# Performance work log

Hardware: AMD Instinct MI355X
Metric: run time of the kernel (lower is better)

Reference implementation:

```python
import jax, jax.numpy as jnp
import numpy as np

B, N, T, D, H, NE = 8, 128, 49, 4, 256, 2  # batch, nodes, timesteps, dims, hidden, edge types


def _mlp(x, w1, b1, w2, b2):
    # NRI-style 2-layer MLP with ELU activations (dropout=0, batch_norm off)
    h = jax.nn.elu(x @ w1 + b1)
    return jax.nn.elu(h @ w2 + b2)


def setup_inputs() -> dict:
    key = jax.random.key(0)
    ks = jax.random.split(key, 11)
    # fully-connected graph without self loops -> E = N*(N-1)
    off = ~np.eye(N, dtype=bool)
    recv_idx, send_idx = np.nonzero(off)
    eye = np.eye(N, dtype=np.float32)
    rec_rel = jnp.asarray(eye[recv_idx])   # [E, N] one-hot receivers
    send_rel = jnp.asarray(eye[send_idx])  # [E, N] one-hot senders
    x = jax.random.normal(ks[0], (B, N, T, D), jnp.float32)

    def lin(k, fi, fo):
        kw, kb = jax.random.split(k)
        return (0.02 * jax.random.normal(kw, (fi, fo), jnp.float32),
                0.02 * jax.random.normal(kb, (fo,), jnp.float32))

    F = T * D
    n1w1, n1b1 = lin(ks[1], F, H)
    n1w2, n1b2 = lin(ks[2], H, H)
    e1w1, e1b1 = lin(ks[3], 2 * H, H)
    e1w2, e1b2 = lin(ks[4], H, H)
    n2w1, n2b1 = lin(ks[5], H, H)
    n2w2, n2b2 = lin(ks[6], H, H)
    e2w1, e2b1 = lin(ks[7], 3 * H, H)
    e2w2, e2b2 = lin(ks[8], H, H)
    ow, ob = lin(ks[9], H, NE)
    return dict(x=x, rec_rel=rec_rel, send_rel=send_rel,
                n1w1=n1w1, n1b1=n1b1, n1w2=n1w2, n1b2=n1b2,
                e1w1=e1w1, e1b1=e1b1, e1w2=e1w2, e1b2=e1b2,
                n2w1=n2w1, n2b1=n2b1, n2w2=n2w2, n2b2=n2b2,
                e2w1=e2w1, e2b1=e2b1, e2w2=e2w2, e2b2=e2b2,
                ow=ow, ob=ob)


def reference(x, rec_rel, send_rel,
              n1w1, n1b1, n1w2, n1b2,
              e1w1, e1b1, e1w2, e1b2,
              n2w1, n2b1, n2w2, n2b2,
              e2w1, e2b1, e2w2, e2b2,
              ow, ob):
    b, n = x.shape[0], x.shape[1]
    h = x.reshape(b, n, -1)                         # [B, N, T*D]
    h = _mlp(h, n1w1, n1b1, n1w2, n1b2)             # node_emd 1 -> [B, N, H]
    r = jnp.einsum('en,bnf->bef', rec_rel, h)       # gather receivers [B, E, H]
    s = jnp.einsum('en,bnf->bef', send_rel, h)      # gather senders  [B, E, H]
    e = _mlp(jnp.concatenate([r, s], -1), e1w1, e1b1, e1w2, e1b2)  # edge_emd 1
    x_skip = e                                      # '@' skip connection
    agg = jnp.einsum('en,bef->bnf', rec_rel, e)     # aggregate sum -> [B, N, H]
    h = _mlp(agg, n2w1, n2b1, n2w2, n2b2)           # node_emd 2
    r = jnp.einsum('en,bnf->bef', rec_rel, h)
    s = jnp.einsum('en,bnf->bef', send_rel, h)
    e = jnp.concatenate([r, s, x_skip], -1)         # pairwise concat + residual cat
    e = _mlp(e, e2w1, e2b1, e2w2, e2b2)             # edge_emd 2 (final)
    return e @ ow + ob                              # [B, E, n_edge_types]
```

## Files before the change

kernel.cpp:

```cpp
#include <hip/hip_runtime.h>
#include <hip/hip_bf16.h>

typedef unsigned short ushort_t;
typedef short bf16x8 __attribute__((ext_vector_type(8)));
typedef float f32x4 __attribute__((ext_vector_type(4)));

#define B_ 8
#define N_ 128
#define E_ 16256
#define BE 130048

__device__ __forceinline__ float eluf(float x) {
    return x > 0.0f ? x : __expf(x) - 1.0f;
}
__device__ __forceinline__ ushort_t f2bf(float f) {
    union { float f; unsigned u; } v; v.f = f;
    return (ushort_t)((v.u + 0x7fffu + ((v.u >> 16) & 1u)) >> 16);
}
__device__ __forceinline__ float bf2f(ushort_t h) {
    union { unsigned u; float f; } v; v.u = ((unsigned)h) << 16;
    return v.f;
}

__device__ __forceinline__ void glds16(void* lds, const void* g) {
    __builtin_amdgcn_global_load_lds(
        (const __attribute__((address_space(1))) unsigned int*)g,
        (__attribute__((address_space(3))) unsigned int*)lds, 16, 0, 0);
}

__device__ __forceinline__ void img32_elem(const float* __restrict__ w,
                                           ushort_t* __restrict__ img, int i) {
    int c = i >> 13;  int r = i & 8191;
    int n = r >> 5;   int jq = r & 31;
    int quad = jq >> 3, j = jq & 7;
    int kc = quad ^ ((n >> 1) & 3);
    int k = c * 32 + kc * 8 + j;
    img[i] = f2bf(w[(size_t)k * 256 + n]);
}
__device__ __forceinline__ void img128_elem(const float* __restrict__ w,
                                            ushort_t* __restrict__ img, int i) {
    int c = i >> 15;  int r = i & 32767;
    int n = r >> 7;   int wdx = r & 127;
    int up = wdx >> 3, j = wdx & 7;
    int u = up ^ (n & 15);
    int k = c * 128 + u * 8 + j;
    img[i] = f2bf(w[(size_t)k * 256 + n]);
}
__device__ __forceinline__ void img128_pad(const float* __restrict__ w,
                                           ushort_t* __restrict__ img, int i, int Kreal) {
    int c = i >> 15;  int r = i & 32767;
    int n = r >> 7;   int wdx = r & 127;
    int up = wdx >> 3, j = wdx & 7;
    int u = up ^ (n & 15);
    int k = c * 128 + u * 8 + j;
    img[i] = (k < Kreal) ? f2bf(w[(size_t)k * 256 + n]) : (ushort_t)0;
}

__global__ __launch_bounds__(256) void wprep_all(
    const float* __restrict__ n1w1, ushort_t* __restrict__ s0,
    const float* __restrict__ n1w2, ushort_t* __restrict__ s1,
    const float* __restrict__ e1w1, ushort_t* __restrict__ s2, ushort_t* __restrict__ s3,
    const float* __restrict__ n2w1, ushort_t* __restrict__ s4,
    const float* __restrict__ n2w2, ushort_t* __restrict__ s5,
    const float* __restrict__ e2w1, ushort_t* __restrict__ s6, ushort_t* __restrict__ s7,
    ushort_t* __restrict__ s8,
    const float* __restrict__ e1w2, ushort_t* __restrict__ s9,
    const float* __restrict__ e2w2, ushort_t* __restrict__ s10)
{
    int gid = blockIdx.x * 256 + threadIdx.x;
    int img = gid >> 16, r = gid & 65535;
    switch (img) {
        case 0:  img128_pad (n1w1, s0, r, 196); break;
        case 1:  img128_elem(n1w2, s1, r); break;
        case 2:  img128_elem(e1w1, s2, r); break;
        case 3:  img128_elem(e1w1 + 65536, s3, r); break;
        case 4:  img128_elem(n2w1, s4, r); break;
        case 5:  img128_elem(n2w2, s5, r); break;
        case 6:  img128_elem(e2w1, s6, r); break;
        case 7:  img128_elem(e2w1 + 65536, s7, r); break;
        case 8:  img32_elem (e2w1 + 131072, s8, r); break;
        case 9:  img32_elem (e1w2, s9, r); break;
        default: img32_elem (e2w2, s10, r); break;
    }
}

template<bool TWOIN>
__global__ __launch_bounds__(256, 1) void node_fused(
    const float* __restrict__ in0, const float* __restrict__ in1,
    const ushort_t* __restrict__ iw1, const float* __restrict__ b1,
    const ushort_t* __restrict__ iw2, const float* __restrict__ b2,
    const ushort_t* __restrict__ ipr, const ushort_t* __restrict__ ips,
    const float* __restrict__ bE,
    float* __restrict__ P)
{
    extern __shared__ char smem[];
    const int t = threadIdx.x;
    const int wid = t >> 6, lane = t & 63, lr = lane & 15, lg = lane >> 4;
    const int r0 = blockIdx.x * 32;

    float bias1[4], bias2[4], biasP[4];
    #pragma unroll
    for (int f = 0; f < 4; ++f) {
        int col = wid * 64 + f * 16 + lr;
        bias1[f] = b1[col];
        bias2[f] = b2[col];
        biasP[f] = 0.5f * bE[col];
    }

    f32x4 acc[2][4];
    #pragma unroll
    for (int m = 0; m < 2; ++m)
        #pragma unroll
        for (int f = 0; f < 4; ++f) acc[m][f] = f32x4{0.f, 0.f, 0.f, 0.f};

    auto stageW = [&](const ushort_t* img, int c, int p) {
        const char* src = (const char*)img + (size_t)c * 65536 + wid * 16384 + lane * 16;
        char* dst = smem + 16384 + p * 65536 + wid * 16384;
        #pragma unroll
        for (int it = 0; it < 16; ++it) glds16(dst + it * 1024, src + it * 1024);
    };

    int cc = 0;
    auto runGemm = [&](const ushort_t* img, const ushort_t* nimg) {
        for (int c = 0; c < 2; ++c) {
            const int p = cc & 1;
            if (c + 1 < 2)  stageW(img, 1, p ^ 1);
            else if (nimg)  stageW(nimg, 0, p ^ 1);
            const char* Wp = smem + 16384 + p * 65536;
            #pragma unroll
            for (int ks = 0; ks < 4; ++ks) {
                const int c32 = c * 4 + ks;
                bf16x8 a[2], b[4];
                const int qh = ((c32 * 4 + lg) ^ (lr & 7)) << 4;
                #pragma unroll
                for (int m = 0; m < 2; ++m)
                    a[m] = *(const bf16x8*)(smem + (m * 16 + lr) * 512 + qh);
                #pragma unroll
                for (int f = 0; f < 4; ++f)
                    b[f] = *(const bf16x8*)(Wp + (wid * 64 + f * 16 + lr) * 256 + (((ks * 4 + lg) ^ lr) << 4));
                #pragma unroll
                for (int m = 0; m < 2; ++m)
                    #pragma unroll
                    for (int f = 0; f < 4; ++f)
                        acc[m][f] = __builtin_amdgcn_mfma_f32_16x16x32_bf16(a[m], b[f], acc[m][f], 0, 0, 0);
            }
            __syncthreads();
            ++cc;
        }
    };

    auto transition = [&](const float* bv) {
        #pragma unroll
        for (int m = 0; m < 2; ++m)
            #pragma unroll
            for (int f = 0; f < 4; ++f) {
                const int col = wid * 64 + f * 16 + lr;
                const int ch = col >> 3;
                #pragma unroll
                for (int r = 0; r < 4; ++r) {
                    const int row = m * 16 + lg * 4 + r;
                    float v = eluf(acc[m][f][r] + bv[f]);
                    *(ushort_t*)(smem + row * 512 + ((ch ^ (row & 7)) << 4) + ((col & 7) << 1)) = f2bf(v);
                }
                acc[m][f] = f32x4{0.f, 0.f, 0.f, 0.f};
            }
        __syncthreads();
    };

    auto pwrite = [&](int half) {
        #pragma unroll
        for (int m = 0; m < 2; ++m)
            #pragma unroll
            for (int f = 0; f < 4; ++f) {
                const int col = wid * 64 + f * 16 + lr;
                #pragma unroll
                for (int r = 0; r < 4; ++r) {
                    const int row = m * 16 + lg * 4 + r;
                    P[(size_t)(r0 + row) * 512 + half * 256 + col] = acc[m][f][r] + biasP[f];
                }
                acc[m][f] = f32x4{0.f, 0.f, 0.f, 0.f};
            }
    };

    stageW(iw1, 0, 0);
    for (int idx = t; idx < 32 * 128; idx += 256) {
        const int row = idx >> 7;
        const int c0 = (idx & 127) * 2;
        float v0, v1;
        if (TWOIN) {
            const float* pa = in0 + (size_t)(r0 + row) * 256;
            const float* pb = in1 + (size_t)(r0 + row) * 256;
            v0 = pa[c0] + pb[c0];
            v1 = pa[c0 + 1] + pb[c0 + 1];
        } else {
            const float* pa = in0 + (size_t)(r0 + row) * 196;
            v0 = (c0 < 196) ? pa[c0] : 0.f;
            v1 = (c0 + 1 < 196) ? pa[c0 + 1] : 0.f;
        }
        unsigned u = (unsigned)f2bf(v0) | ((unsigned)f2bf(v1) << 16);
        const int ch = c0 >> 3;
        *(unsigned*)(smem + row * 512 + ((ch ^ (row & 7)) << 4) + (c0 & 7) * 2) = u;
    }
    __syncthreads();

    runGemm(iw1, iw2);
    transition(bias1);
    runGemm(iw2, ipr);
    transition(bias2);
    runGemm(ipr, ips);
    pwrite(0);
    runGemm(ips, nullptr);
    pwrite(1);
}

__global__ __launch_bounds__(512, 2) void edge1_kernel(
    const float* __restrict__ P1,
    const ushort_t* __restrict__ wAimg, const float* __restrict__ biasA,
    const ushort_t* __restrict__ wBimg,
    ushort_t* __restrict__ G1,
    float* __restrict__ aggp0, float* __restrict__ aggp1)
{
    extern __shared__ char smem[];
    const int t = threadIdx.x;
    const int wid = t >> 6, lane = t & 63, lr = lane & 15, lg = lane >> 4;
    const int wr = wid >> 1, wc = wid & 1;
    const int q4 = (lg ^ ((lr >> 1) & 3)) << 4;
    const int blockRow = blockIdx.x * 256;

    auto stageW = [&](const ushort_t* img, int c, int p) {
        const char* src = (const char*)img + (size_t)c * 16384 + wid * 2048 + lane * 16;
        char* dst = smem + 131072 + p * 16384 + wid * 2048;
        glds16(dst, src);
        glds16(dst + 1024, src + 1024);
    };

    float bA[8];
    #pragma unroll
    for (int f = 0; f < 8; ++f) bA[f] = biasA[wc * 128 + f * 16 + lr];

    f32x4 acc[4][8];
    #pragma unroll
    for (int m = 0; m < 4; ++m)
        #pragma unroll
        for (int f = 0; f < 8; ++f) acc[m][f] = f32x4{0.f, 0.f, 0.f, 0.f};

    stageW(wAimg, 0, 0);
    #pragma unroll 4
    for (int j = 0; j < 32; ++j) {
        const int row = wid * 32 + j;
        const int rg = blockRow + row;
        const int b = rg / E_; const int e = rg - b * E_;
        const int rcv = e / 127; const int kk = e - rcv * 127;
        const int snd = kk + (kk >= rcv ? 1 : 0);
        const float4 vr = *(const float4*)(P1 + (size_t)(b * N_ + rcv) * 512 + lane * 4);
        const float4 vs = *(const float4*)(P1 + (size_t)(b * N_ + snd) * 512 + 256 + lane * 4);
        unsigned u0 = (unsigned)f2bf(eluf(vr.x + vs.x)) | ((unsigned)f2bf(eluf(vr.y + vs.y)) << 16);
        unsigned u1 = (unsigned)f2bf(eluf(vr.z + vs.z)) | ((unsigned)f2bf(eluf(vr.w + vs.w)) << 16);
        const int byte = row * 512 + ((((lane >> 1) ^ (row & 7))) << 4) + (lane & 1) * 8;
        *(uint2*)(smem + byte) = make_uint2(u0, u1);
    }
    __syncthreads();

    for (int c = 0; c < 8; ++c) {
        const int p = c & 1;
        if (c < 7) stageW(wAimg, c + 1, p ^ 1);
        else       stageW(wBimg, 0, p ^ 1);
        const char* Wp = smem + 131072 + p * 16384;
        bf16x8 a[4], b[8];
        const int qh = ((c * 4 + lg) ^ (lr & 7)) << 4;
        #pragma unroll
        for (int m = 0; m < 4; ++m)
            a[m] = *(const bf16x8*)(smem + (wr * 64 + m * 16 + lr) * 512 + qh);
        #pragma unroll
        for (int f = 0; f < 8; ++f)
            b[f] = *(const bf16x8*)(Wp + (wc * 128 + f * 16 + lr) * 64 + q4);
        #pragma unroll
        for (int m = 0; m < 4; ++m)
            #pragma unroll
            for (int f = 0; f < 8; ++f)
                acc[m][f] = __builtin_amdgcn_mfma_f32_16x16x32_bf16(a[m], b[f], acc[m][f], 0, 0, 0);
        __syncthreads();
    }

    const int gR0 = blockRow + wr * 64;
    const int sFirst = gR0 / 127;
    const int bk = 127 - (gR0 - sFirst * 127);
    float s0[8], s1[8];
    #pragma unroll
    for (int f = 0; f < 8; ++f) { s0[f] = 0.f; s1[f] = 0.f; }
    #pragma unroll
    for (int m = 0; m < 4; ++m)
        #pragma unroll
        for (int f = 0; f < 8; ++f) {
            const int col = wc * 128 + f * 16 + lr;
            const int ch = col >> 3;
            #pragma unroll
            for (int r = 0; r < 4; ++r) {
                const int rowL = m * 16 + lg * 4 + r;
                const int row = wr * 64 + rowL;
                float v = eluf(acc[m][f][r] + bA[f]);
                *(ushort_t*)(smem + row * 512 + ((ch ^ (row & 7)) << 4) + ((col & 7) << 1)) = f2bf(v);
                if (rowL < bk) s0[f] += v; else s1[f] += v;
            }
            acc[m][f] = f32x4{0.f, 0.f, 0.f, 0.f};
        }
    #pragma unroll
    for (int f = 0; f < 8; ++f) {
        s0[f] += __shfl_xor(s0[f], 16); s0[f] += __shfl_xor(s0[f], 32);
        s1[f] += __shfl_xor(s1[f], 16); s1[f] += __shfl_xor(s1[f], 32);
    }
    float* pt = (float*)(smem + 131072 + 16384);
    if (lg == 0) {
        #pragma unroll
        for (int f = 0; f < 8; ++f) {
            pt[(wid * 2 + 0) * 128 + f * 16 + lr] = s0[f];
            pt[(wid * 2 + 1) * 128 + f * 16 + lr] = s1[f];
        }
    }
    __syncthreads();
    {
        const int S0 = blockRow / 127;
        const int last = (blockRow + 255) / 127;
        const int cnt = last - S0 + 1;
        for (int task = t; task < cnt * 256; task += 512) {
            const int k = task >> 8;
            const int col = task & 255;
            const int sigma = S0 + k;
            const int wcq = col >> 7, c128 = col & 127;
            float sum = 0.f;
            #pragma unroll
            for (int w2r = 0; w2r < 4; ++w2r) {
                int sf = (blockRow + w2r * 64) / 127;
                int jj = sigma - sf;
                if (jj == 0 || jj == 1)
                    sum += pt[((w2r * 2 + wcq) * 2 + jj) * 128 + c128];
            }
            const bool startIn = (127 * sigma >= blockRow);
            const bool endIn = (127 * sigma + 127 <= blockRow + 256);
            if (startIn) {
                aggp0[(size_t)sigma * 256 + col] = sum;
                if (endIn) aggp1[(size_t)sigma * 256 + col] = 0.f;
            } else {
                aggp1[(size_t)sigma * 256 + col] = sum;
            }
        }
    }
    __syncthreads();

    for (int c = 0; c < 8; ++c) {
        const int p = c & 1;
        if (c < 7) stageW(wBimg, c + 1, p ^ 1);
        const char* Wp = smem + 131072 + p * 16384;
        bf16x8 a[4], b[8];
        const int qh = ((c * 4 + lg) ^ (lr & 7)) << 4;
        #pragma unroll
        for (int m = 0; m < 4; ++m)
            a[m] = *(const bf16x8*)(smem + (wr * 64 + m * 16 + lr) * 512 + qh);
        #pragma unroll
        for (int f = 0; f < 8; ++f)
            b[f] = *(const bf16x8*)(Wp + (wc * 128 + f * 16 + lr) * 64 + q4);
        #pragma unroll
        for (int m = 0; m < 4; ++m)
            #pragma unroll
            for (int f = 0; f < 8; ++f)
                acc[m][f] = __builtin_amdgcn_mfma_f32_16x16x32_bf16(a[m], b[f], acc[m][f], 0, 0, 0);
        __syncthreads();
    }

    char* slice = smem + wid * 16384;
    #pragma unroll
    for (int m = 0; m < 4; ++m)
        #pragma unroll
        for (int f = 0; f < 8; ++f) {
            const int col = f * 16 + lr;
            const int cch = col >> 3;
            #pragma unroll
            for (int r = 0; r < 4; ++r) {
                const int rowL = m * 16 + lg * 4 + r;
                *(ushort_t*)(slice + rowL * 256 + ((cch ^ (rowL & 7)) << 4) + ((col & 7) << 1)) =
                    f2bf(acc[m][f][r]);
            }
        }
    asm volatile("s_waitcnt lgkmcnt(0)" ::: "memory");
    #pragma unroll
    for (int it = 0; it < 16; ++it) {
        const int q = it * 64 + lane;
        const int row = q >> 4, ccp = q & 15;
        bf16x8 v = *(const bf16x8*)(slice + row * 256 + (ccp << 4));
        const int cch = ccp ^ (row & 7);
        const int grow = blockRow + wr * 64 + row;
        *(bf16x8*)(G1 + (size_t)grow * 256 + wc * 128 + cch * 8) = v;
    }
}

__global__ __launch_bounds__(512, 2) void edge2_kernel(
    const ushort_t* __restrict__ G1, const float* __restrict__ P2,
    const ushort_t* __restrict__ wCimg, const float* __restrict__ bC,
    const float* __restrict__ ow, const float* __restrict__ ob,
    float* __restrict__ out)
{
    extern __shared__ char smem[];
    const int t = threadIdx.x;
    const int wid = t >> 6, lane = t & 63, lr = lane & 15, lg = lane >> 4;
    const int wr = wid >> 1, wc = wid & 1;
    const int q4 = (lg ^ ((lr >> 1) & 3)) << 4;
    const int blockRow = blockIdx.x * 256;

    auto stageW = [&](int c, int p) {
        const char* src = (const char*)wCimg + (size_t)c * 16384 + wid * 2048 + lane * 16;
        char* dst = smem + 131072 + p * 16384 + wid * 2048;
        glds16(dst, src);
        glds16(dst + 1024, src + 1024);
    };

    float biasC[8];
    #pragma unroll
    for (int f = 0; f < 8; ++f) biasC[f] = bC[wc * 128 + f * 16 + lr];

    f32x4 acc[4][8];
    #pragma unroll
    for (int m = 0; m < 4; ++m)
        #pragma unroll
        for (int f = 0; f < 8; ++f) acc[m][f] = f32x4{0.f, 0.f, 0.f, 0.f};

    stageW(0, 0);
    #pragma unroll 4
    for (int j = 0; j < 32; ++j) {
        const int row = wid * 32 + j;
        const int rg = blockRow + row;
        const int b = rg / E_; const int e = rg - b * E_;
        const int rcv = e / 127; const int kk = e - rcv * 127;
        const int snd = kk + (kk >= rcv ? 1 : 0);
        const ushort4 g4 = *(const ushort4*)(G1 + (size_t)rg * 256 + lane * 4);
        const float4 vr = *(const float4*)(P2 + (size_t)(b * N_ + rcv) * 512 + lane * 4);
        const float4 vs = *(const float4*)(P2 + (size_t)(b * N_ + snd) * 512 + 256 + lane * 4);
        unsigned u0 = (unsigned)f2bf(eluf(bf2f(g4.x) + vr.x + vs.x))
                    | ((unsigned)f2bf(eluf(bf2f(g4.y) + vr.y + vs.y)) << 16);
        unsigned u1 = (unsigned)f2bf(eluf(bf2f(g4.z) + vr.z + vs.z))
                    | ((unsigned)f2bf(eluf(bf2f(g4.w) + vr.w + vs.w)) << 16);
        const int byte = row * 512 + ((((lane >> 1) ^ (row & 7))) << 4) + (lane & 1) * 8;
        *(uint2*)(smem + byte) = make_uint2(u0, u1);
    }
    __syncthreads();

    for (int c = 0; c < 8; ++c) {
        const int p = c & 1;
        if (c < 7) stageW(c + 1, p ^ 1);
        const char* Wp = smem + 131072 + p * 16384;
        bf16x8 a[4], b[8];
        const int qh = ((c * 4 + lg) ^ (lr & 7)) << 4;
        #pragma unroll
        for (int m = 0; m < 4; ++m)
            a[m] = *(const bf16x8*)(smem + (wr * 64 + m * 16 + lr) * 512 + qh);
        #pragma unroll
        for (int f = 0; f < 8; ++f)
            b[f] = *(const bf16x8*)(Wp + (wc * 128 + f * 16 + lr) * 64 + q4);
        #pragma unroll
        for (int m = 0; m < 4; ++m)
            #pragma unroll
            for (int f = 0; f < 8; ++f)
                acc[m][f] = __builtin_amdgcn_mfma_f32_16x16x32_bf16(a[m], b[f], acc[m][f], 0, 0, 0);
        __syncthreads();
    }

    float ow0[8], ow1[8];
    #pragma unroll
    for (int f = 0; f < 8; ++f) {
        int col = wc * 128 + f * 16 + lr;
        ow0[f] = ow[col * 2 + 0];
        ow1[f] = ow[col * 2 + 1];
    }
    float s0[4][4], s1[4][4];
    #pragma unroll
    for (int m = 0; m < 4; ++m)
        #pragma unroll
        for (int r = 0; r < 4; ++r) { s0[m][r] = 0.f; s1[m][r] = 0.f; }
    #pragma unroll
    for (int m = 0; m < 4; ++m)
        #pragma unroll
        for (int f = 0; f < 8; ++f)
            #pragma unroll
            for (int r = 0; r < 4; ++r) {
                float v = eluf(acc[m][f][r] + biasC[f]);
                s0[m][r] = fmaf(v, ow0[f], s0[m][r]);
                s1[m][r] = fmaf(v, ow1[f], s1[m][r]);
            }
    #pragma unroll
    for (int msk = 1; msk <= 8; msk <<= 1)
        #pragma unroll
        for (int m = 0; m < 4; ++m)
            #pragma unroll
            for (int r = 0; r < 4; ++r) {
                s0[m][r] += __shfl_xor(s0[m][r], msk);
                s1[m][r] += __shfl_xor(s1[m][r], msk);
            }
    float* part = (float*)smem;
    if (lr == 0) {
        #pragma unroll
        for (int m = 0; m < 4; ++m)
            #pragma unroll
            for (int r = 0; r < 4; ++r) {
                const int row = wr * 64 + m * 16 + lg * 4 + r;
                part[(row * 2 + 0) * 2 + wc] = s0[m][r];
                part[(row * 2 + 1) * 2 + wc] = s1[m][r];
            }
    }
    __syncthreads();
    const int row = t >> 1, chn = t & 1;
    float val = part[(row * 2 + chn) * 2 + 0] + part[(row * 2 + chn) * 2 + 1] + ob[chn];
    out[(size_t)(blockRow + row) * 2 + chn] = val;
}

extern "C" void kernel_launch(void* const* d_in, const int* in_sizes, int n_in,
                              void* d_out, int out_size, void* d_ws, size_t ws_size,
                              hipStream_t stream)
{
    const float* x    = (const float*)d_in[0];
    const float* n1w1 = (const float*)d_in[3];
    const float* n1b1 = (const float*)d_in[4];
    const float* n1w2 = (const float*)d_in[5];
    const float* n1b2 = (const float*)d_in[6];
    const float* e1w1 = (const float*)d_in[7];
    const float* e1b1 = (const float*)d_in[8];
    const float* e1w2 = (const float*)d_in[9];
    const float* e1b2 = (const float*)d_in[10];
    const float* n2w1 = (const float*)d_in[11];
    const float* n2b1 = (const float*)d_in[12];
    const float* n2w2 = (const float*)d_in[13];
    const float* n2b2 = (const float*)d_in[14];
    const float* e2w1 = (const float*)d_in[15];
    const float* e2b1 = (const float*)d_in[16];
    const float* e2w2 = (const float*)d_in[17];
    const float* e2b2 = (const float*)d_in[18];
    const float* ow   = (const float*)d_in[19];
    const float* ob   = (const float*)d_in[20];

    char* ws = (char*)d_ws;
    const size_t KB = 1024;
    ushort_t* i_n1w1 = (ushort_t*)(ws + 0 * 128 * KB);
    ushort_t* i_n1w2 = (ushort_t*)(ws + 1 * 128 * KB);
    ushort_t* i_p1r  = (ushort_t*)(ws + 2 * 128 * KB);
    ushort_t* i_p1s  = (ushort_t*)(ws + 3 * 128 * KB);
    ushort_t* i_n2w1 = (ushort_t*)(ws + 4 * 128 * KB);
    ushort_t* i_n2w2 = (ushort_t*)(ws + 5 * 128 * KB);
    ushort_t* i_p2r  = (ushort_t*)(ws + 6 * 128 * KB);
    ushort_t* i_p2s  = (ushort_t*)(ws + 7 * 128 * KB);
    ushort_t* wB     = (ushort_t*)(ws + 8 * 128 * KB);
    ushort_t* wA     = (ushort_t*)(ws + 9 * 128 * KB);
    ushort_t* wC     = (ushort_t*)(ws + 10 * 128 * KB);
    float*    P1    = (float*)(ws + 1536 * KB);
    float*    P2    = (float*)(ws + 1536 * KB + (2u << 20));
    float*    aggp0 = (float*)(ws + 1536 * KB + (4u << 20));
    float*    aggp1 = (float*)(ws + 1536 * KB + (5u << 20));
    ushort_t* G1    = (ushort_t*)(ws + 1536 * KB + (6u << 20));

    float* out = (float*)d_out;

    hipFuncSetAttribute((const void*)node_fused<false>,
                        hipFuncAttributeMaxDynamicSharedMemorySize, 147456);
    hipFuncSetAttribute((const void*)node_fused<true>,
                        hipFuncAttributeMaxDynamicSharedMemorySize, 147456);
    hipFuncSetAttribute((const void*)edge1_kernel,
                        hipFuncAttributeMaxDynamicSharedMemorySize, 163840);
    hipFuncSetAttribute((const void*)edge2_kernel,
                        hipFuncAttributeMaxDynamicSharedMemorySize, 163840);

    wprep_all<<<2816, 256, 0, stream>>>(
        n1w1, i_n1w1, n1w2, i_n1w2, e1w1, i_p1r, i_p1s,
        n2w1, i_n2w1, n2w2, i_n2w2, e2w1, i_p2r, i_p2s, wB,
        e1w2, wA, e2w2, wC);

    node_fused<false><<<32, 256, 147456, stream>>>(
        x, nullptr, i_n1w1, n1b1, i_n1w2, n1b2, i_p1r, i_p1s, e1b1, P1);

    edge1_kernel<<<BE / 256, 512, 163840, stream>>>(
        P1, wA, e1b2, wB, G1, aggp0, aggp1);

    node_fused<true><<<32, 256, 147456, stream>>>(
        aggp0, aggp1, i_n2w1, n2b1, i_n2w2, n2b2, i_p2r, i_p2s, e2b1, P2);

    edge2_kernel<<<BE / 256, 512, 163840, stream>>>(
        G1, P2, wC, e2b2, ow, ob, out);
}
```

Before: 161.6 us.

## Replace double-buffered 32-wide weight chunks with single-buffered 64-wide chunks in edge kernels

The edge GEMMs that stream weights from global memory now stage a 64-deep K chunk (32 KB) into one LDS buffer per iteration, and each thread loads four 16-byte slices instead of two. This replaces the previous double-buffered 32-deep chunks, and the weight image layout and swizzle change to match. The change halves the number of loop iterations and barriers, but it gives up overlap between the weight loads and the MFMA work, because each chunk is loaded and then waited on before it is used. The prologue no longer prefetches weights during the activation staging, and the scratch pointer used for the reduction moves to the freed buffer.

```diff
diff --git a/kernel.cpp b/kernel.cpp
--- a/kernel.cpp
+++ b/kernel.cpp
@@ -28,13 +28,13 @@
         (__attribute__((address_space(3))) unsigned int*)lds, 16, 0, 0);
 }
 
-__device__ __forceinline__ void img32_elem(const float* __restrict__ w,
+__device__ __forceinline__ void img64_elem(const float* __restrict__ w,
                                            ushort_t* __restrict__ img, int i) {
-    int c = i >> 13;  int r = i & 8191;
-    int n = r >> 5;   int jq = r & 31;
-    int quad = jq >> 3, j = jq & 7;
-    int kc = quad ^ ((n >> 1) & 3);
-    int k = c * 32 + kc * 8 + j;
+    int c = i >> 14;  int r = i & 16383;
+    int n = r >> 6;   int wdx = r & 63;
+    int up = wdx >> 3, j = wdx & 7;
+    int u = up ^ (n & 7);
+    int k = c * 64 + u * 8 + j;
     img[i] = f2bf(w[(size_t)k * 256 + n]);
 }
 __device__ __forceinline__ void img128_elem(const float* __restrict__ w,
@@ -78,9 +78,9 @@
         case 5:  img128_elem(n2w2, s5, r); break;
         case 6:  img128_elem(e2w1, s6, r); break;
         case 7:  img128_elem(e2w1 + 65536, s7, r); break;
-        case 8:  img32_elem (e2w1 + 131072, s8, r); break;
-        case 9:  img32_elem (e1w2, s9, r); break;
-        default: img32_elem (e2w2, s10, r); break;
+        case 8:  img64_elem (e2w1 + 131072, s8, r); break;
+        case 9:  img64_elem (e1w2, s9, r); break;
+        default: img64_elem (e2w2, s10, r); break;
     }
 }
 
@@ -224,14 +224,13 @@
     const int t = threadIdx.x;
     const int wid = t >> 6, lane = t & 63, lr = lane & 15, lg = lane >> 4;
     const int wr = wid >> 1, wc = wid & 1;
-    const int q4 = (lg ^ ((lr >> 1) & 3)) << 4;
     const int blockRow = blockIdx.x * 256;
 
-    auto stageW = [&](const ushort_t* img, int c, int p) {
-        const char* src = (const char*)img + (size_t)c * 16384 + wid * 2048 + lane * 16;
-        char* dst = smem + 131072 + p * 16384 + wid * 2048;
-        glds16(dst, src);
-        glds16(dst + 1024, src + 1024);
+    auto stageW64 = [&](const ushort_t* img, int c) {
+        const char* src = (const char*)img + (size_t)c * 32768 + wid * 4096 + lane * 16;
+        char* dst = smem + 131072 + wid * 4096;
+        #pragma unroll
+        for (int it = 0; it < 4; ++it) glds16(dst + it * 1024, src + it * 1024);
     };
 
     float bA[8];
@@ -244,7 +243,6 @@
         #pragma unroll
         for (int f = 0; f < 8; ++f) acc[m][f] = f32x4{0.f, 0.f, 0.f, 0.f};
 
-    stageW(wAimg, 0, 0);
     #pragma unroll 4
     for (int j = 0; j < 32; ++j) {
         const int row = wid * 32 + j;
@@ -259,26 +257,29 @@
         const int byte = row * 512 + ((((lane >> 1) ^ (row & 7))) << 4) + (lane & 1) * 8;
         *(uint2*)(smem + byte) = make_uint2(u0, u1);
     }
-    __syncthreads();
-
-    for (int c = 0; c < 8; ++c) {
-        const int p = c & 1;
-        if (c < 7) stageW(wAimg, c + 1, p ^ 1);
-        else       stageW(wBimg, 0, p ^ 1);
-        const char* Wp = smem + 131072 + p * 16384;
-        bf16x8 a[4], b[8];
-        const int qh = ((c * 4 + lg) ^ (lr & 7)) << 4;
-        #pragma unroll
-        for (int m = 0; m < 4; ++m)
-            a[m] = *(const bf16x8*)(smem + (wr * 64 + m * 16 + lr) * 512 + qh);
-        #pragma unroll
-        for (int f = 0; f < 8; ++f)
-            b[f] = *(const bf16x8*)(Wp + (wc * 128 + f * 16 + lr) * 64 + q4);
-        #pragma unroll
-        for (int m = 0; m < 4; ++m)
+
+    for (int c = 0; c < 4; ++c) {
+        stageW64(wAimg, c);
+        __syncthreads();
+        const char* Wp = smem + 131072;
+        #pragma unroll
+        for (int ks = 0; ks < 2; ++ks) {
+            const int kk = c * 2 + ks;
+            bf16x8 a[4], b[8];
+            const int qh = ((kk * 4 + lg) ^ (lr & 7)) << 4;
+            const int sb = ((ks * 4 + lg) ^ (lr & 7)) << 4;
+            #pragma unroll
+            for (int m = 0; m < 4; ++m)
+                a[m] = *(const bf16x8*)(smem + (wr * 64 + m * 16 + lr) * 512 + qh);
             #pragma unroll
             for (int f = 0; f < 8; ++f)
-                acc[m][f] = __builtin_amdgcn_mfma_f32_16x16x32_bf16(a[m], b[f], acc[m][f], 0, 0, 0);
+                b[f] = *(const bf16x8*)(Wp + (wc * 128 + f * 16 + lr) * 128 + sb);
+            #pragma unroll
+            for (int m = 0; m < 4; ++m)
+                #pragma unroll
+                for (int f = 0; f < 8; ++f)
+                    acc[m][f] = __builtin_amdgcn_mfma_f32_16x16x32_bf16(a[m], b[f], acc[m][f], 0, 0, 0);
+        }
         __syncthreads();
     }
 
@@ -309,7 +310,7 @@
         s0[f] += __shfl_xor(s0[f], 16); s0[f] += __shfl_xor(s0[f], 32);
         s1[f] += __shfl_xor(s1[f], 16); s1[f] += __shfl_xor(s1[f], 32);
     }
-    float* pt = (float*)(smem + 131072 + 16384);
+    float* pt = (float*)(smem + 131072);
     if (lg == 0) {
         #pragma unroll
         for (int f = 0; f < 8; ++f) {
@@ -347,23 +348,28 @@
     }
     __syncthreads();
 
-    for (int c = 0; c < 8; ++c) {
-        const int p = c & 1;
-        if (c < 7) stageW(wBimg, c + 1, p ^ 1);
-        const char* Wp = smem + 131072 + p * 16384;
-        bf16x8 a[4], b[8];
-        const int qh = ((c * 4 + lg) ^ (lr & 7)) << 4;
-        #pragma unroll
-        for (int m = 0; m < 4; ++m)
-            a[m] = *(const bf16x8*)(smem + (wr * 64 + m * 16 + lr) * 512 + qh);
-        #pragma unroll
-        for (int f = 0; f < 8; ++f)
-            b[f] = *(const bf16x8*)(Wp + (wc * 128 + f * 16 + lr) * 64 + q4);
-        #pragma unroll
-        for (int m = 0; m < 4; ++m)
+    for (int c = 0; c < 4; ++c) {
+        stageW64(wBimg, c);
+        __syncthreads();
+        const char* Wp = smem + 131072;
+        #pragma unroll
+        for (int ks = 0; ks < 2; ++ks) {
+            const int kk = c * 2 + ks;
+            bf16x8 a[4], b[8];
+            const int qh = ((kk * 4 + lg) ^ (lr & 7)) << 4;
+            const int sb = ((ks * 4 + lg) ^ (lr & 7)) << 4;
+            #pragma unroll
+            for (int m = 0; m < 4; ++m)
+                a[m] = *(const bf16x8*)(smem + (wr * 64 + m * 16 + lr) * 512 + qh);
             #pragma unroll
             for (int f = 0; f < 8; ++f)
-                acc[m][f] = __builtin_amdgcn_mfma_f32_16x16x32_bf16(a[m], b[f], acc[m][f], 0, 0, 0);
+                b[f] = *(const bf16x8*)(Wp + (wc * 128 + f * 16 + lr) * 128 + sb);
+            #pragma unroll
+            for (int m = 0; m < 4; ++m)
+                #pragma unroll
+                for (int f = 0; f < 8; ++f)
+                    acc[m][f] = __builtin_amdgcn_mfma_f32_16x16x32_bf16(a[m], b[f], acc[m][f], 0, 0, 0);
+        }
         __syncthreads();
     }
 
@@ -403,14 +409,13 @@
     const int t = threadIdx.x;
     const int wid = t >> 6, lane = t & 63, lr = lane & 15, lg = lane >> 4;
     const int wr = wid >> 1, wc = wid & 1;
-    const int q4 = (lg ^ ((lr >> 1) & 3)) << 4;
     const int blockRow = blockIdx.x * 256;
 
-    auto stageW = [&](int c, int p) {
-        const char* src = (const char*)wCimg + (size_t)c * 16384 + wid * 2048 + lane * 16;
-        char* dst = smem + 131072 + p * 16384 + wid * 2048;
-        glds16(dst, src);
-        glds16(dst + 1024, src + 1024);
+    auto stageW64 = [&](int c) {
+        const char* src = (const char*)wCimg + (size_t)c * 32768 + wid * 4096 + lane * 16;
+        char* dst = smem + 131072 + wid * 4096;
+        #pragma unroll
+        for (int it = 0; it < 4; ++it) glds16(dst + it * 1024, src + it * 1024);
     };
 
     float biasC[8];
@@ -423,7 +428,6 @@
         #pragma unroll
         for (int f = 0; f < 8; ++f) acc[m][f] = f32x4{0.f, 0.f, 0.f, 0.f};
 
-    stageW(0, 0);
     #pragma unroll 4
     for (int j = 0; j < 32; ++j) {
         const int row = wid * 32 + j;
@@ -441,25 +445,29 @@
         const int byte = row * 512 + ((((lane >> 1) ^ (row & 7))) << 4) + (lane & 1) * 8;
         *(uint2*)(smem + byte) = make_uint2(u0, u1);
     }
-    __syncthreads();
-
-    for (int c = 0; c < 8; ++c) {
-        const int p = c & 1;
-        if (c < 7) stageW(c + 1, p ^ 1);
-        const char* Wp = smem + 131072 + p * 16384;
-        bf16x8 a[4], b[8];
-        const int qh = ((c * 4 + lg) ^ (lr & 7)) << 4;
-        #pragma unroll
-        for (int m = 0; m < 4; ++m)
-            a[m] = *(const bf16x8*)(smem + (wr * 64 + m * 16 + lr) * 512 + qh);
-        #pragma unroll
-        for (int f = 0; f < 8; ++f)
-            b[f] = *(const bf16x8*)(Wp + (wc * 128 + f * 16 + lr) * 64 + q4);
-        #pragma unroll
-        for (int m = 0; m < 4; ++m)
+
+    for (int c = 0; c < 4; ++c) {
+        stageW64(c);
+        __syncthreads();
+        const char* Wp = smem + 131072;
+        #pragma unroll
+        for (int ks = 0; ks < 2; ++ks) {
+            const int kk = c * 2 + ks;
+            bf16x8 a[4], b[8];
+            const int qh = ((kk * 4 + lg) ^ (lr & 7)) << 4;
+            const int sb = ((ks * 4 + lg) ^ (lr & 7)) << 4;
+            #pragma unroll
+            for (int m = 0; m < 4; ++m)
+                a[m] = *(const bf16x8*)(smem + (wr * 64 + m * 16 + lr) * 512 + qh);
             #pragma unroll
             for (int f = 0; f < 8; ++f)
-                acc[m][f] = __builtin_amdgcn_mfma_f32_16x16x32_bf16(a[m], b[f], acc[m][f], 0, 0, 0);
+                b[f] = *(const bf16x8*)(Wp + (wc * 128 + f * 16 + lr) * 128 + sb);
+            #pragma unroll
+            for (int m = 0; m < 4; ++m)
+                #pragma unroll
+                for (int f = 0; f < 8; ++f)
+                    acc[m][f] = __builtin_amdgcn_mfma_f32_16x16x32_bf16(a[m], b[f], acc[m][f], 0, 0, 0);
+        }
         __syncthreads();
     }
 
```

After: 181.0 us. 12.0% more time.

## Load edge-GEMM weight fragments straight into registers instead of LDS staging

Applied to the files above, without the earlier changes.

The edge kernels stop staging weight chunks into double-buffered LDS with per-chunk barriers. Each wave now loads its B fragments directly from global memory (L2-resident) into registers, two chunks ahead, using a plain unswizzled k-contiguous weight image. This drops eight block-wide syncs per GEMM and shrinks dynamic LDS, at the cost of more VGPRs and exposed global-load latency.

```diff
diff --git a/kernel.cpp b/kernel.cpp
--- a/kernel.cpp
+++ b/kernel.cpp
@@ -28,14 +28,11 @@
         (__attribute__((address_space(3))) unsigned int*)lds, 16, 0, 0);
 }
 
-__device__ __forceinline__ void img32_elem(const float* __restrict__ w,
-                                           ushort_t* __restrict__ img, int i) {
+__device__ __forceinline__ void img32p_elem(const float* __restrict__ w,
+                                            ushort_t* __restrict__ img, int i) {
     int c = i >> 13;  int r = i & 8191;
-    int n = r >> 5;   int jq = r & 31;
-    int quad = jq >> 3, j = jq & 7;
-    int kc = quad ^ ((n >> 1) & 3);
-    int k = c * 32 + kc * 8 + j;
-    img[i] = f2bf(w[(size_t)k * 256 + n]);
+    int n = r >> 5;   int kk = r & 31;
+    img[i] = f2bf(w[(size_t)(c * 32 + kk) * 256 + n]);
 }
 __device__ __forceinline__ void img128_elem(const float* __restrict__ w,
                                             ushort_t* __restrict__ img, int i) {
@@ -78,9 +75,9 @@
         case 5:  img128_elem(n2w2, s5, r); break;
         case 6:  img128_elem(e2w1, s6, r); break;
         case 7:  img128_elem(e2w1 + 65536, s7, r); break;
-        case 8:  img32_elem (e2w1 + 131072, s8, r); break;
-        case 9:  img32_elem (e1w2, s9, r); break;
-        default: img32_elem (e2w2, s10, r); break;
+        case 8:  img32p_elem(e2w1 + 131072, s8, r); break;
+        case 9:  img32p_elem(e1w2, s9, r); break;
+        default: img32p_elem(e2w2, s10, r); break;
     }
 }
 
@@ -224,27 +221,46 @@
     const int t = threadIdx.x;
     const int wid = t >> 6, lane = t & 63, lr = lane & 15, lg = lane >> 4;
     const int wr = wid >> 1, wc = wid & 1;
-    const int q4 = (lg ^ ((lr >> 1) & 3)) << 4;
     const int blockRow = blockIdx.x * 256;
-
-    auto stageW = [&](const ushort_t* img, int c, int p) {
-        const char* src = (const char*)img + (size_t)c * 16384 + wid * 2048 + lane * 16;
-        char* dst = smem + 131072 + p * 16384 + wid * 2048;
-        glds16(dst, src);
-        glds16(dst + 1024, src + 1024);
+    const int boff = (wc * 128 + lr) * 32 + lg * 8;
+
+    float bA[8];
+    #pragma unroll
+    for (int f = 0; f < 8; ++f) bA[f] = biasA[wc * 128 + f * 16 + lr];
+
+    f32x4 acc[4][8];
+    #pragma unroll
+    for (int m = 0; m < 4; ++m)
+        #pragma unroll
+        for (int f = 0; f < 8; ++f) acc[m][f] = f32x4{0.f, 0.f, 0.f, 0.f};
+
+    auto gemmReg = [&](const ushort_t* wimg) {
+        const ushort_t* wb = wimg + boff;
+        bf16x8 brg[2][8];
+        #pragma unroll
+        for (int f = 0; f < 8; ++f) brg[0][f] = *(const bf16x8*)(wb + 0 * 8192 + f * 512);
+        #pragma unroll
+        for (int f = 0; f < 8; ++f) brg[1][f] = *(const bf16x8*)(wb + 1 * 8192 + f * 512);
+        #pragma unroll
+        for (int c = 0; c < 8; ++c) {
+            bf16x8 a[4];
+            const int qh = ((c * 4 + lg) ^ (lr & 7)) << 4;
+            #pragma unroll
+            for (int m = 0; m < 4; ++m)
+                a[m] = *(const bf16x8*)(smem + (wr * 64 + m * 16 + lr) * 512 + qh);
+            #pragma unroll
+            for (int m = 0; m < 4; ++m)
+                #pragma unroll
+                for (int f = 0; f < 8; ++f)
+                    acc[m][f] = __builtin_amdgcn_mfma_f32_16x16x32_bf16(a[m], brg[c & 1][f], acc[m][f], 0, 0, 0);
+            if (c + 2 < 8) {
+                #pragma unroll
+                for (int f = 0; f < 8; ++f)
+                    brg[c & 1][f] = *(const bf16x8*)(wb + (size_t)(c + 2) * 8192 + f * 512);
+            }
+        }
     };
 
-    float bA[8];
-    #pragma unroll
-    for (int f = 0; f < 8; ++f) bA[f] = biasA[wc * 128 + f * 16 + lr];
-
-    f32x4 acc[4][8];
-    #pragma unroll
-    for (int m = 0; m < 4; ++m)
-        #pragma unroll
-        for (int f = 0; f < 8; ++f) acc[m][f] = f32x4{0.f, 0.f, 0.f, 0.f};
-
-    stageW(wAimg, 0, 0);
     #pragma unroll 4
     for (int j = 0; j < 32; ++j) {
         const int row = wid * 32 + j;
@@ -261,26 +277,8 @@
     }
     __syncthreads();
 
-    for (int c = 0; c < 8; ++c) {
-        const int p = c & 1;
-        if (c < 7) stageW(wAimg, c + 1, p ^ 1);
-        else       stageW(wBimg, 0, p ^ 1);
-        const char* Wp = smem + 131072 + p * 16384;
-        bf16x8 a[4], b[8];
-        const int qh = ((c * 4 + lg) ^ (lr & 7)) << 4;
-        #pragma unroll
-        for (int m = 0; m < 4; ++m)
-            a[m] = *(const bf16x8*)(smem + (wr * 64 + m * 16 + lr) * 512 + qh);
-        #pragma unroll
-        for (int f = 0; f < 8; ++f)
-            b[f] = *(const bf16x8*)(Wp + (wc * 128 + f * 16 + lr) * 64 + q4);
-        #pragma unroll
-        for (int m = 0; m < 4; ++m)
-            #pragma unroll
-            for (int f = 0; f < 8; ++f)
-                acc[m][f] = __builtin_amdgcn_mfma_f32_16x16x32_bf16(a[m], b[f], acc[m][f], 0, 0, 0);
-        __syncthreads();
-    }
+    gemmReg(wAimg);
+    __syncthreads();
 
     const int gR0 = blockRow + wr * 64;
     const int sFirst = gR0 / 127;
@@ -309,7 +307,7 @@
         s0[f] += __shfl_xor(s0[f], 16); s0[f] += __shfl_xor(s0[f], 32);
         s1[f] += __shfl_xor(s1[f], 16); s1[f] += __shfl_xor(s1[f], 32);
     }
-    float* pt = (float*)(smem + 131072 + 16384);
+    float* pt = (float*)(smem + 131072);
     if (lg == 0) {
         #pragma unroll
         for (int f = 0; f < 8; ++f) {
@@ -345,27 +343,9 @@
             }
         }
     }
-    __syncthreads();
-
-    for (int c = 0; c < 8; ++c) {
-        const int p = c & 1;
-        if (c < 7) stageW(wBimg, c + 1, p ^ 1);
-        const char* Wp = smem + 131072 + p * 16384;
-        bf16x8 a[4], b[8];
-        const int qh = ((c * 4 + lg) ^ (lr & 7)) << 4;
-        #pragma unroll
-        for (int m = 0; m < 4; ++m)
-            a[m] = *(const bf16x8*)(smem + (wr * 64 + m * 16 + lr) * 512 + qh);
-        #pragma unroll
-        for (int f = 0; f < 8; ++f)
-            b[f] = *(const bf16x8*)(Wp + (wc * 128 + f * 16 + lr) * 64 + q4);
-        #pragma unroll
-        for (int m = 0; m < 4; ++m)
-            #pragma unroll
-            for (int f = 0; f < 8; ++f)
-                acc[m][f] = __builtin_amdgcn_mfma_f32_16x16x32_bf16(a[m], b[f], acc[m][f], 0, 0, 0);
-        __syncthreads();
-    }
+
+    gemmReg(wBimg);
+    __syncthreads();
 
     char* slice = smem + wid * 16384;
     #pragma unroll
@@ -403,15 +383,8 @@
     const int t = threadIdx.x;
     const int wid = t >> 6, lane = t & 63, lr = lane & 15, lg = lane >> 4;
     const int wr = wid >> 1, wc = wid & 1;
-    const int q4 = (lg ^ ((lr >> 1) & 3)) << 4;
     const int blockRow = blockIdx.x * 256;
-
-    auto stageW = [&](int c, int p) {
-        const char* src = (const char*)wCimg + (size_t)c * 16384 + wid * 2048 + lane * 16;
-        char* dst = smem + 131072 + p * 16384 + wid * 2048;
-        glds16(dst, src);
-        glds16(dst + 1024, src + 1024);
-    };
+    const int boff = (wc * 128 + lr) * 32 + lg * 8;
 
     float biasC[8];
     #pragma unroll
@@ -423,7 +396,6 @@
         #pragma unroll
         for (int f = 0; f < 8; ++f) acc[m][f] = f32x4{0.f, 0.f, 0.f, 0.f};
 
-    stageW(0, 0);
     #pragma unroll 4
     for (int j = 0; j < 32; ++j) {
         const int row = wid * 32 + j;
@@ -443,25 +415,33 @@
     }
     __syncthreads();
 
-    for (int c = 0; c < 8; ++c) {
-        const int p = c & 1;
-        if (c < 7) stageW(c + 1, p ^ 1);
-        const char* Wp = smem + 131072 + p * 16384;
-        bf16x8 a[4], b[8];
-        const int qh = ((c * 4 + lg) ^ (lr & 7)) << 4;
-        #pragma unroll
-        for (int m = 0; m < 4; ++m)
-            a[m] = *(const bf16x8*)(smem + (wr * 64 + m * 16 + lr) * 512 + qh);
-        #pragma unroll
-        for (int f = 0; f < 8; ++f)
-            b[f] = *(const bf16x8*)(Wp + (wc * 128 + f * 16 + lr) * 64 + q4);
-        #pragma unroll
-        for (int m = 0; m < 4; ++m)
-            #pragma unroll
-            for (int f = 0; f < 8; ++f)
-                acc[m][f] = __builtin_amdgcn_mfma_f32_16x16x32_bf16(a[m], b[f], acc[m][f], 0, 0, 0);
-        __syncthreads();
-    }
+    {
+        const ushort_t* wb = wCimg + boff;
+        bf16x8 brg[2][8];
+        #pragma unroll
+        for (int f = 0; f < 8; ++f) brg[0][f] = *(const bf16x8*)(wb + 0 * 8192 + f * 512);
+        #pragma unroll
+        for (int f = 0; f < 8; ++f) brg[1][f] = *(const bf16x8*)(wb + 1 * 8192 + f * 512);
+        #pragma unroll
+        for (int c = 0; c < 8; ++c) {
+            bf16x8 a[4];
+            const int qh = ((c * 4 + lg) ^ (lr & 7)) << 4;
+            #pragma unroll
+            for (int m = 0; m < 4; ++m)
+                a[m] = *(const bf16x8*)(smem + (wr * 64 + m * 16 + lr) * 512 + qh);
+            #pragma unroll
+            for (int m = 0; m < 4; ++m)
+                #pragma unroll
+                for (int f = 0; f < 8; ++f)
+                    acc[m][f] = __builtin_amdgcn_mfma_f32_16x16x32_bf16(a[m], brg[c & 1][f], acc[m][f], 0, 0, 0);
+            if (c + 2 < 8) {
+                #pragma unroll
+                for (int f = 0; f < 8; ++f)
+                    brg[c & 1][f] = *(const bf16x8*)(wb + (size_t)(c + 2) * 8192 + f * 512);
+            }
+        }
+    }
+    __syncthreads();
 
     float ow0[8], ow1[8];
     #pragma unroll
@@ -561,9 +541,9 @@
     hipFuncSetAttribute((const void*)node_fused<true>,
                         hipFuncAttributeMaxDynamicSharedMemorySize, 147456);
     hipFuncSetAttribute((const void*)edge1_kernel,
-                        hipFuncAttributeMaxDynamicSharedMemorySize, 163840);
+                        hipFuncAttributeMaxDynamicSharedMemorySize, 139264);
     hipFuncSetAttribute((const void*)edge2_kernel,
-                        hipFuncAttributeMaxDynamicSharedMemorySize, 163840);
+                        hipFuncAttributeMaxDynamicSharedMemorySize, 131072);
 
     wprep_all<<<2816, 256, 0, stream>>>(
         n1w1, i_n1w1, n1w2, i_n1w2, e1w1, i_p1r, i_p1s,
@@ -573,12 +553,12 @@
     node_fused<false><<<32, 256, 147456, stream>>>(
         x, nullptr, i_n1w1, n1b1, i_n1w2, n1b2, i_p1r, i_p1s, e1b1, P1);
 
-    edge1_kernel<<<BE / 256, 512, 163840, stream>>>(
+    edge1_kernel<<<BE / 256, 512, 139264, stream>>>(
         P1, wA, e1b2, wB, G1, aggp0, aggp1);
 
     node_fused<true><<<32, 256, 147456, stream>>>(
         aggp0, aggp1, i_n2w1, n2b1, i_n2w2, n2b2, i_p2r, i_p2s, e2b1, P2);
 
-    edge2_kernel<<<BE / 256, 512, 163840, stream>>>(
+    edge2_kernel<<<BE / 256, 512, 131072, stream>>>(
         G1, P2, wC, e2b2, ow, ob, out);
 }
```

Result: slower. 175.7 us (+8.7%).
